# Performance work log

Hardware: AMD Instinct MI355X
Metric: run time of the kernel (lower is better)

## Reference

```python
import jax, jax.numpy as jnp
import numpy as np

B, T, D, K = 64, 512, 1024, 10
TEMP = 0.07
EPS = 1e-8


def setup_inputs() -> dict:
    key = jax.random.key(0)
    features = jax.random.normal(key, (B, T, D), dtype=jnp.float32)
    # Replicate torch.randperm-based negative sampling: for each batch b,
    # sample K indices without replacement from the (B-1)*T vectors of all
    # other batches, then map flat index -> (batch, time).
    rng = np.random.default_rng(0)
    neg_b = np.empty((B, K), dtype=np.int64)
    neg_t = np.empty((B, K), dtype=np.int64)
    for b in range(B):
        idx = rng.permutation((B - 1) * T)[:K]
        bb = idx // T
        bb = bb + (bb >= b)  # skip own batch
        neg_b[b] = bb
        neg_t[b] = idx % T
    return {"features": features, "neg_b": jnp.asarray(neg_b), "neg_t": jnp.asarray(neg_t)}


def _unit(x):
    # torch F.cosine_similarity semantics: divide by max(||x||, eps)
    n = jnp.sqrt(jnp.sum(x * x, axis=-1, keepdims=True))
    return x / jnp.maximum(n, EPS)


def reference(features, neg_b, neg_t):
    anchors = features[:, 1:T - 1, :]     # [B, T-2, D]
    positives = features[:, 2:T, :]       # [B, T-2, D]
    a_hat = _unit(anchors)
    pos_sim = jnp.sum(a_hat * _unit(positives), axis=-1) / TEMP          # [B, T-2]
    negs = jax.lax.stop_gradient(features)[neg_b, neg_t]                  # [B, K, D]
    sim_neg = jnp.einsum('btd,bkd->btk', a_hat, _unit(negs)) / TEMP       # [B, T-2, K]
    exp_pos = jnp.exp(pos_sim)
    exp_neg = jnp.exp(sim_neg).sum(axis=-1)
    loss = -jnp.log(exp_pos / (exp_pos + exp_neg))                        # [B, T-2]
    return loss.mean(axis=1).mean()
```

## Files before the change

kernel.cpp:

```cpp
#include <hip/hip_runtime.h>

typedef unsigned int uint;

#define B_ 64
#define T_ 512
#define K_ 10
constexpr float TEMP_ = 0.07f;
constexpr float EPS_ = 1e-8f;
constexpr int F4ROW = 256;
constexpr int APW = 8;
constexpr int NBLK = 16;
constexpr int ROWU = 512;

__device__ __forceinline__ float dot4(float4 a, float4 b) {
    return a.x * b.x + a.y * b.y + a.z * b.z + a.w * b.w;
}
__device__ __forceinline__ float plo_(uint u){ return __uint_as_float(u << 16); }
__device__ __forceinline__ float phi_(uint u){ return __uint_as_float(u & 0xffff0000u); }
__device__ __forceinline__ uint bfr_(float f){
    uint u = __float_as_uint(f);
    return (u + 0x7fffu + ((u >> 16) & 1u)) >> 16;
}
__device__ __forceinline__ uint pack2_(float lo, float hi){ return bfr_(lo) | (bfr_(hi) << 16); }

template <int CTRL>
__device__ __forceinline__ float dpp_add(float x){
    int y = __builtin_amdgcn_update_dpp(0, __float_as_int(x), CTRL, 0xf, 0xf, false);
    return x + __int_as_float(y);
}
__device__ __forceinline__ float red64(float x){
    x = dpp_add<0x128>(x);
    x = dpp_add<0x124>(x);
    x = dpp_add<0x122>(x);
    x = dpp_add<0x121>(x);
    int y = __builtin_amdgcn_ds_swizzle(__float_as_int(x), 0x401F);
    x += __int_as_float(y);
    x += __shfl_xor(x, 32, 64);
    return x;
}

__global__ __launch_bounds__(64) void signcl_prep(
    const float* __restrict__ features,
    const int* __restrict__ neg_b,
    const int* __restrict__ neg_t,
    uint* __restrict__ negs_pk)
{
    const int blk = blockIdx.x;
    const int b = blk / K_, k = blk % K_;
    const int l = threadIdx.x;

    const int nb = neg_b[b * K_ + k];
    const int nt = neg_t[b * K_ + k];
    const float4* rp = reinterpret_cast<const float4*>(features)
                       + ((size_t)nb * T_ + nt) * F4ROW + l * 4;
    float4 v0 = rp[0], v1 = rp[1], v2 = rp[2], v3 = rp[3];
    float ss = dot4(v0, v0) + dot4(v1, v1) + dot4(v2, v2) + dot4(v3, v3);
    ss = red64(ss);
    const float inv = 1.f / fmaxf(sqrtf(ss), EPS_);

    uint4* out = reinterpret_cast<uint4*>(negs_pk + ((size_t)b * K_ + k) * ROWU);
    uint4 o;
    o.x = pack2_(v0.x * inv, v0.y * inv);
    o.y = pack2_(v0.z * inv, v0.w * inv);
    o.z = pack2_(v1.x * inv, v1.y * inv);
    o.w = pack2_(v1.z * inv, v1.w * inv);
    out[l] = o;
    o.x = pack2_(v2.x * inv, v2.y * inv);
    o.y = pack2_(v2.z * inv, v2.w * inv);
    o.z = pack2_(v3.x * inv, v3.y * inv);
    o.w = pack2_(v3.z * inv, v3.w * inv);
    out[64 + l] = o;
}

__global__ __launch_bounds__(256) void signcl_main(
    const float* __restrict__ features,
    const uint* __restrict__ negs_pk,
    float* __restrict__ partials)
{
    __shared__ uint s_negs[K_ * ROWU];
    __shared__ float s_part[4];

    const int tid = threadIdx.x;
    const int l = tid & 63, w = tid >> 6;
    const int bid = blockIdx.x;
    const int b = bid >> 4;
    const int c = bid & (NBLK - 1);

    {
        const uint4* gsrc = reinterpret_cast<const uint4*>(negs_pk + (size_t)b * K_ * ROWU);
        uint4* sdst = reinterpret_cast<uint4*>(s_negs);
#pragma unroll
        for (int j = 0; j < 5; ++j) sdst[tid + j * 256] = gsrc[tid + j * 256];
    }
    __syncthreads();

    const float4* fb = reinterpret_cast<const float4*>(features) + (size_t)b * T_ * F4ROW;
    const uint4* n4 = reinterpret_cast<const uint4*>(s_negs);
    const int ta = 1 + c * 32 + w * APW;

    const float4* rA = fb + (size_t)ta * F4ROW + l * 4;
    const float4* rN = fb + (size_t)min(ta + 1, T_ - 1) * F4ROW + l * 4;
    float4 A0 = rA[0], A1 = rA[1], A2 = rA[2], A3 = rA[3];
    float4 N0 = rN[0], N1 = rN[1], N2 = rN[2], N3 = rN[3];
    float ssc = dot4(A0, A0) + dot4(A1, A1) + dot4(A2, A2) + dot4(A3, A3);
    float inv_c = 1.f / fmaxf(sqrtf(red64(ssc)), EPS_);

    const float invT = 1.f / TEMP_;
    float lsum = 0.f;

#pragma unroll
    for (int i = 0; i < APW; ++i){
        const int t = ta + i;
        const int tp = (t + 2 < T_) ? (t + 2) : (T_ - 1);
        const float4* rP = fb + (size_t)tp * F4ROW + l * 4;
        float4 P0 = rP[0], P1 = rP[1], P2 = rP[2], P3 = rP[3];

        float nd[K_];
#pragma unroll
        for (int k = 0; k < K_; ++k){
            uint4 u0 = n4[k * 128 + l];
            uint4 u1 = n4[k * 128 + 64 + l];
            float a;
            a = fmaf(A0.x, plo_(u0.x), 0.f);
            a = fmaf(A0.y, phi_(u0.x), a);
            a = fmaf(A0.z, plo_(u0.y), a);
            a = fmaf(A0.w, phi_(u0.y), a);
            a = fmaf(A1.x, plo_(u0.z), a);
            a = fmaf(A1.y, phi_(u0.z), a);
            a = fmaf(A1.z, plo_(u0.w), a);
            a = fmaf(A1.w, phi_(u0.w), a);
            a = fmaf(A2.x, plo_(u1.x), a);
            a = fmaf(A2.y, phi_(u1.x), a);
            a = fmaf(A2.z, plo_(u1.y), a);
            a = fmaf(A2.w, phi_(u1.y), a);
            a = fmaf(A3.x, plo_(u1.z), a);
            a = fmaf(A3.y, phi_(u1.z), a);
            a = fmaf(A3.z, plo_(u1.w), a);
            a = fmaf(A3.w, phi_(u1.w), a);
            nd[k] = a;
        }
#pragma unroll
        for (int k = 0; k < K_; ++k) nd[k] = red64(nd[k]);

        float ssn = dot4(N0, N0) + dot4(N1, N1) + dot4(N2, N2) + dot4(N3, N3);
        float dp  = dot4(A0, N0) + dot4(A1, N1) + dot4(A2, N2) + dot4(A3, N3);
        ssn = red64(ssn);
        dp  = red64(dp);
        const float inv_n = 1.f / fmaxf(sqrtf(ssn), EPS_);

        if (t <= T_ - 2){
            float pos = dp * inv_c * inv_n * invT;
            float sc = inv_c * invT;
            float se = 0.f;
#pragma unroll
            for (int k = 0; k < K_; ++k) se += __expf(nd[k] * sc);
            lsum += __logf(__expf(pos) + se) - pos;
        }
        A0 = N0; A1 = N1; A2 = N2; A3 = N3; inv_c = inv_n;
        N0 = P0; N1 = P1; N2 = P2; N3 = P3;
    }

    if (l == 0) s_part[w] = lsum;
    __syncthreads();
    if (tid == 0) partials[bid] = s_part[0] + s_part[1] + s_part[2] + s_part[3];
}

__global__ __launch_bounds__(256) void signcl_reduce(
    const float* __restrict__ partials, float* __restrict__ out)
{
    __shared__ float s_w[4];
    const int tid = threadIdx.x;
    float s = 0.f;
    for (int idx = tid; idx < B_ * NBLK; idx += 256) s += partials[idx];
#pragma unroll
    for (int m = 32; m >= 1; m >>= 1) s += __shfl_xor(s, m, 64);
    const int w = tid >> 6, lane = tid & 63;
    if (lane == 0) s_w[w] = s;
    __syncthreads();
    if (tid == 0) {
        float t = s_w[0] + s_w[1] + s_w[2] + s_w[3];
        out[0] = t / (float)(B_ * (T_ - 2));
    }
}

extern "C" void kernel_launch(void* const* d_in, const int* in_sizes, int n_in,
                              void* d_out, int out_size, void* d_ws, size_t ws_size,
                              hipStream_t stream) {
    const float* features = (const float*)d_in[0];
    const int* neg_b = (const int*)d_in[1];
    const int* neg_t = (const int*)d_in[2];
    uint* negs_pk = (uint*)d_ws;
    float* partials = (float*)((char*)d_ws + (2u << 20));

    signcl_prep<<<B_ * K_, 64, 0, stream>>>(features, neg_b, neg_t, negs_pk);
    signcl_main<<<B_ * NBLK, 256, 0, stream>>>(features, negs_pk, partials);
    signcl_reduce<<<1, 256, 0, stream>>>(partials, (float*)d_out);
}
```

Measured before the change: 45.03 us.

## Use fp16 dot2 for negatives, process two anchors per LDS pass, DPP row reductions

Negatives are now stored as fp16 (round-toward-zero pack) rather than bf16, and anchors are packed to fp16 so the negative dot products use v_dot2 instructions. Each loop iteration handles two anchors, so every LDS read of a negative is reused twice. The cross-lane reductions switch to DPP row broadcasts, leaving the full sum in lane 63, which removes the swizzle and shuffle steps. Occupancy is hinted with launch_bounds(256,2). In exchange, fp16 products lose precision, and holding more rows live raises register pressure.

```diff
diff --git a/kernel.cpp b/kernel.cpp
--- a/kernel.cpp
+++ b/kernel.cpp
@@ -1,6 +1,7 @@
 #include <hip/hip_runtime.h>
 
 typedef unsigned int uint;
+typedef _Float16 f16x2 __attribute__((ext_vector_type(2)));
 
 #define B_ 64
 #define T_ 512
@@ -15,28 +16,31 @@
 __device__ __forceinline__ float dot4(float4 a, float4 b) {
     return a.x * b.x + a.y * b.y + a.z * b.z + a.w * b.w;
 }
-__device__ __forceinline__ float plo_(uint u){ return __uint_as_float(u << 16); }
-__device__ __forceinline__ float phi_(uint u){ return __uint_as_float(u & 0xffff0000u); }
-__device__ __forceinline__ uint bfr_(float f){
-    uint u = __float_as_uint(f);
-    return (u + 0x7fffu + ((u >> 16) & 1u)) >> 16;
-}
-__device__ __forceinline__ uint pack2_(float lo, float hi){ return bfr_(lo) | (bfr_(hi) << 16); }
+__device__ __forceinline__ f16x2 bc_(uint u){ return __builtin_bit_cast(f16x2, u); }
+__device__ __forceinline__ f16x2 pkrtz(float a, float b){
+    return __builtin_bit_cast(f16x2, __builtin_amdgcn_cvt_pkrtz(a, b));
+}
+__device__ __forceinline__ uint pkrtz_u(float a, float b){
+    return __builtin_bit_cast(uint, __builtin_amdgcn_cvt_pkrtz(a, b));
+}
 
 template <int CTRL>
 __device__ __forceinline__ float dpp_add(float x){
     int y = __builtin_amdgcn_update_dpp(0, __float_as_int(x), CTRL, 0xf, 0xf, false);
     return x + __int_as_float(y);
 }
-__device__ __forceinline__ float red64(float x){
+__device__ __forceinline__ float red6(float x){
     x = dpp_add<0x128>(x);
     x = dpp_add<0x124>(x);
     x = dpp_add<0x122>(x);
     x = dpp_add<0x121>(x);
-    int y = __builtin_amdgcn_ds_swizzle(__float_as_int(x), 0x401F);
-    x += __int_as_float(y);
-    x += __shfl_xor(x, 32, 64);
+    x = dpp_add<0x142>(x);
+    x = dpp_add<0x143>(x);
     return x;
+}
+__device__ __forceinline__ float red64(float x){
+    x = red6(x);
+    return __shfl(x, 63, 64);
 }
 
 __global__ __launch_bounds__(64) void signcl_prep(
@@ -60,19 +64,29 @@
 
     uint4* out = reinterpret_cast<uint4*>(negs_pk + ((size_t)b * K_ + k) * ROWU);
     uint4 o;
-    o.x = pack2_(v0.x * inv, v0.y * inv);
-    o.y = pack2_(v0.z * inv, v0.w * inv);
-    o.z = pack2_(v1.x * inv, v1.y * inv);
-    o.w = pack2_(v1.z * inv, v1.w * inv);
+    o.x = pkrtz_u(v0.x * inv, v0.y * inv);
+    o.y = pkrtz_u(v0.z * inv, v0.w * inv);
+    o.z = pkrtz_u(v1.x * inv, v1.y * inv);
+    o.w = pkrtz_u(v1.z * inv, v1.w * inv);
     out[l] = o;
-    o.x = pack2_(v2.x * inv, v2.y * inv);
-    o.y = pack2_(v2.z * inv, v2.w * inv);
-    o.z = pack2_(v3.x * inv, v3.y * inv);
-    o.w = pack2_(v3.z * inv, v3.w * inv);
+    o.x = pkrtz_u(v2.x * inv, v2.y * inv);
+    o.y = pkrtz_u(v2.z * inv, v2.w * inv);
+    o.z = pkrtz_u(v3.x * inv, v3.y * inv);
+    o.w = pkrtz_u(v3.z * inv, v3.w * inv);
     out[64 + l] = o;
 }
 
-__global__ __launch_bounds__(256) void signcl_main(
+#define PACK8(F, X0, X1, X2, X3)                              \
+    F##0 = pkrtz(X0.x, X0.y);                                 \
+    F##1 = pkrtz(X0.z, X0.w);                                 \
+    F##2 = pkrtz(X1.x, X1.y);                                 \
+    F##3 = pkrtz(X1.z, X1.w);                                 \
+    F##4 = pkrtz(X2.x, X2.y);                                 \
+    F##5 = pkrtz(X2.z, X2.w);                                 \
+    F##6 = pkrtz(X3.x, X3.y);                                 \
+    F##7 = pkrtz(X3.z, X3.w);
+
+__global__ __launch_bounds__(256, 2) void signcl_main(
     const float* __restrict__ features,
     const uint* __restrict__ negs_pk,
     float* __restrict__ partials)
@@ -99,68 +113,91 @@
     const int ta = 1 + c * 32 + w * APW;
 
     const float4* rA = fb + (size_t)ta * F4ROW + l * 4;
-    const float4* rN = fb + (size_t)min(ta + 1, T_ - 1) * F4ROW + l * 4;
+    const float4* rB = fb + (size_t)min(ta + 1, T_ - 1) * F4ROW + l * 4;
+    const float4* rC = fb + (size_t)min(ta + 2, T_ - 1) * F4ROW + l * 4;
     float4 A0 = rA[0], A1 = rA[1], A2 = rA[2], A3 = rA[3];
-    float4 N0 = rN[0], N1 = rN[1], N2 = rN[2], N3 = rN[3];
-    float ssc = dot4(A0, A0) + dot4(A1, A1) + dot4(A2, A2) + dot4(A3, A3);
-    float inv_c = 1.f / fmaxf(sqrtf(red64(ssc)), EPS_);
+    float4 B0 = rB[0], B1 = rB[1], B2 = rB[2], B3 = rB[3];
+    float4 C0 = rC[0], C1 = rC[1], C2 = rC[2], C3 = rC[3];
+
+    f16x2 FA0, FA1, FA2, FA3, FA4, FA5, FA6, FA7;
+    f16x2 FB0, FB1, FB2, FB3, FB4, FB5, FB6, FB7;
+    PACK8(FA, A0, A1, A2, A3);
+    float ssA = dot4(A0, A0) + dot4(A1, A1) + dot4(A2, A2) + dot4(A3, A3);
+    float invA = 1.f / fmaxf(sqrtf(red6(ssA)), EPS_);
 
     const float invT = 1.f / TEMP_;
     float lsum = 0.f;
 
 #pragma unroll
-    for (int i = 0; i < APW; ++i){
-        const int t = ta + i;
-        const int tp = (t + 2 < T_) ? (t + 2) : (T_ - 1);
-        const float4* rP = fb + (size_t)tp * F4ROW + l * 4;
-        float4 P0 = rP[0], P1 = rP[1], P2 = rP[2], P3 = rP[3];
-
-        float nd[K_];
+    for (int j = 0; j < APW / 2; ++j){
+        const int u = ta + 2 * j;
+
+        float4 P0, P1, P2, P3, Q0, Q1, Q2, Q3;
+        if (j < APW / 2 - 1){
+            const float4* rP = fb + (size_t)min(u + 3, T_ - 1) * F4ROW + l * 4;
+            const float4* rQ = fb + (size_t)min(u + 4, T_ - 1) * F4ROW + l * 4;
+            P0 = rP[0]; P1 = rP[1]; P2 = rP[2]; P3 = rP[3];
+            Q0 = rQ[0]; Q1 = rQ[1]; Q2 = rQ[2]; Q3 = rQ[3];
+        }
+
+        PACK8(FB, B0, B1, B2, B3);
+
+        float ndu[K_], ndv[K_];
 #pragma unroll
         for (int k = 0; k < K_; ++k){
             uint4 u0 = n4[k * 128 + l];
             uint4 u1 = n4[k * 128 + 64 + l];
-            float a;
-            a = fmaf(A0.x, plo_(u0.x), 0.f);
-            a = fmaf(A0.y, phi_(u0.x), a);
-            a = fmaf(A0.z, plo_(u0.y), a);
-            a = fmaf(A0.w, phi_(u0.y), a);
-            a = fmaf(A1.x, plo_(u0.z), a);
-            a = fmaf(A1.y, phi_(u0.z), a);
-            a = fmaf(A1.z, plo_(u0.w), a);
-            a = fmaf(A1.w, phi_(u0.w), a);
-            a = fmaf(A2.x, plo_(u1.x), a);
-            a = fmaf(A2.y, phi_(u1.x), a);
-            a = fmaf(A2.z, plo_(u1.y), a);
-            a = fmaf(A2.w, phi_(u1.y), a);
-            a = fmaf(A3.x, plo_(u1.z), a);
-            a = fmaf(A3.y, phi_(u1.z), a);
-            a = fmaf(A3.z, plo_(u1.w), a);
-            a = fmaf(A3.w, phi_(u1.w), a);
-            nd[k] = a;
-        }
-#pragma unroll
-        for (int k = 0; k < K_; ++k) nd[k] = red64(nd[k]);
-
-        float ssn = dot4(N0, N0) + dot4(N1, N1) + dot4(N2, N2) + dot4(N3, N3);
-        float dp  = dot4(A0, N0) + dot4(A1, N1) + dot4(A2, N2) + dot4(A3, N3);
-        ssn = red64(ssn);
-        dp  = red64(dp);
-        const float inv_n = 1.f / fmaxf(sqrtf(ssn), EPS_);
-
-        if (t <= T_ - 2){
-            float pos = dp * inv_c * inv_n * invT;
-            float sc = inv_c * invT;
+            float su = 0.f, sv = 0.f;
+            f16x2 e;
+            e = bc_(u0.x); su = __builtin_amdgcn_fdot2(FA0, e, su, false); sv = __builtin_amdgcn_fdot2(FB0, e, sv, false);
+            e = bc_(u0.y); su = __builtin_amdgcn_fdot2(FA1, e, su, false); sv = __builtin_amdgcn_fdot2(FB1, e, sv, false);
+            e = bc_(u0.z); su = __builtin_amdgcn_fdot2(FA2, e, su, false); sv = __builtin_amdgcn_fdot2(FB2, e, sv, false);
+            e = bc_(u0.w); su = __builtin_amdgcn_fdot2(FA3, e, su, false); sv = __builtin_amdgcn_fdot2(FB3, e, sv, false);
+            e = bc_(u1.x); su = __builtin_amdgcn_fdot2(FA4, e, su, false); sv = __builtin_amdgcn_fdot2(FB4, e, sv, false);
+            e = bc_(u1.y); su = __builtin_amdgcn_fdot2(FA5, e, su, false); sv = __builtin_amdgcn_fdot2(FB5, e, sv, false);
+            e = bc_(u1.z); su = __builtin_amdgcn_fdot2(FA6, e, su, false); sv = __builtin_amdgcn_fdot2(FB6, e, sv, false);
+            e = bc_(u1.w); su = __builtin_amdgcn_fdot2(FA7, e, su, false); sv = __builtin_amdgcn_fdot2(FB7, e, sv, false);
+            ndu[k] = su; ndv[k] = sv;
+        }
+
+        float ssB  = dot4(B0, B0) + dot4(B1, B1) + dot4(B2, B2) + dot4(B3, B3);
+        float ssC  = dot4(C0, C0) + dot4(C1, C1) + dot4(C2, C2) + dot4(C3, C3);
+        float dpAB = dot4(A0, B0) + dot4(A1, B1) + dot4(A2, B2) + dot4(A3, B3);
+        float dpBC = dot4(B0, C0) + dot4(B1, C1) + dot4(B2, C2) + dot4(B3, C3);
+
+#pragma unroll
+        for (int k = 0; k < K_; ++k){ ndu[k] = red6(ndu[k]); ndv[k] = red6(ndv[k]); }
+        ssB = red6(ssB); ssC = red6(ssC); dpAB = red6(dpAB); dpBC = red6(dpBC);
+        const float invB = 1.f / fmaxf(sqrtf(ssB), EPS_);
+        const float invC = 1.f / fmaxf(sqrtf(ssC), EPS_);
+
+        if (u <= T_ - 2){
+            float pos = dpAB * invA * invB * invT;
+            float sc = invA * invT;
             float se = 0.f;
 #pragma unroll
-            for (int k = 0; k < K_; ++k) se += __expf(nd[k] * sc);
+            for (int k = 0; k < K_; ++k) se += __expf(ndu[k] * sc);
             lsum += __logf(__expf(pos) + se) - pos;
         }
-        A0 = N0; A1 = N1; A2 = N2; A3 = N3; inv_c = inv_n;
-        N0 = P0; N1 = P1; N2 = P2; N3 = P3;
+        if (u + 1 <= T_ - 2){
+            float pos = dpBC * invB * invC * invT;
+            float sc = invB * invT;
+            float se = 0.f;
+#pragma unroll
+            for (int k = 0; k < K_; ++k) se += __expf(ndv[k] * sc);
+            lsum += __logf(__expf(pos) + se) - pos;
+        }
+
+        if (j < APW / 2 - 1){
+            PACK8(FA, C0, C1, C2, C3);
+            A0 = C0; A1 = C1; A2 = C2; A3 = C3;
+            B0 = P0; B1 = P1; B2 = P2; B3 = P3;
+            C0 = Q0; C1 = Q1; C2 = Q2; C3 = Q3;
+            invA = invC;
+        }
     }
 
-    if (l == 0) s_part[w] = lsum;
+    if (l == 63) s_part[w] = lsum;
     __syncthreads();
     if (tid == 0) partials[bid] = s_part[0] + s_part[1] + s_part[2] + s_part[3];
 }
```

New measurement: 44.67 us. No clear change (-0.8%).
